# Performance work log

Hardware: AMD Instinct MI355X
Metric: run time of the kernel (lower is better)

## Reference

```python
import jax, jax.numpy as jnp
import numpy as np

N = 50000
E = 400000
IN_DIM = 256
HID = 64
HEADS = 8
OUT_DIM = 40
NEG_SLOPE = 0.2  # PyG GATConv leaky-relu slope


def gat_conv(x, src, dst, W, a_src, a_dst, bias, concat):
    """One PyG-style GATConv (eval mode, self-loops already appended).
    x: [N, in], W: [in, H*C], a_src/a_dst: [H, C], bias: [H*C] or [C]."""
    H, C = a_src.shape
    h = (x @ W).reshape(N, H, C)                       # [N, H, C]
    # per-node attention logits, gathered per edge
    e_src = (h * a_src[None]).sum(-1)                  # [N, H]
    e_dst = (h * a_dst[None]).sum(-1)                  # [N, H]
    alpha = jax.nn.leaky_relu(e_src[src] + e_dst[dst], NEG_SLOPE)  # [Etot, H]
    # segment softmax over incoming edges of each dst node
    amax = jax.ops.segment_max(alpha, dst, num_segments=N)         # [N, H]
    ex = jnp.exp(alpha - amax[dst])
    denom = jax.ops.segment_sum(ex, dst, num_segments=N)           # [N, H]
    coef = ex / denom[dst]                                         # [Etot, H]
    # weighted scatter-add of neighbor features
    msg = h[src] * coef[:, :, None]                                # [Etot, H, C]
    out = jax.ops.segment_sum(msg, dst, num_segments=N)            # [N, H, C]
    out = out.reshape(N, H * C) if concat else out.mean(axis=1)
    return out + bias


def setup_inputs() -> dict:
    key = jax.random.key(0)
    ks = jax.random.split(key, 10)
    x = jax.random.normal(ks[0], (N, IN_DIM), dtype=jnp.float32)
    edge_index = jax.random.randint(ks[1], (2, E), 0, N, dtype=jnp.int32)
    g1 = 1.0 / np.sqrt(IN_DIM)
    g2 = 1.0 / np.sqrt(HID * HEADS)
    W1 = jax.random.normal(ks[2], (IN_DIM, HEADS * HID), dtype=jnp.float32) * g1
    a_src1 = jax.random.normal(ks[3], (HEADS, HID), dtype=jnp.float32) * 0.1
    a_dst1 = jax.random.normal(ks[4], (HEADS, HID), dtype=jnp.float32) * 0.1
    b1 = jnp.zeros((HEADS * HID,), dtype=jnp.float32)
    W2 = jax.random.normal(ks[5], (HEADS * HID, OUT_DIM), dtype=jnp.float32) * g2
    a_src2 = jax.random.normal(ks[6], (1, OUT_DIM), dtype=jnp.float32) * 0.1
    a_dst2 = jax.random.normal(ks[7], (1, OUT_DIM), dtype=jnp.float32) * 0.1
    b2 = jnp.zeros((OUT_DIM,), dtype=jnp.float32)
    return {"x": x, "edge_index": edge_index, "W1": W1, "a_src1": a_src1,
            "a_dst1": a_dst1, "b1": b1, "W2": W2, "a_src2": a_src2,
            "a_dst2": a_dst2, "b2": b2}


def reference(x, edge_index, W1, a_src1, a_dst1, b1, W2, a_src2, a_dst2, b2):
    # append self loops (PyG GATConv default add_self_loops=True)
    loop = jnp.arange(N, dtype=edge_index.dtype)
    src = jnp.concatenate([edge_index[0], loop])
    dst = jnp.concatenate([edge_index[1], loop])
    h = gat_conv(x, src, dst, W1, a_src1, a_dst1, b1, concat=True)
    h = jax.nn.elu(h)
    # dropout is identity in eval mode
    out = gat_conv(h, src, dst, W2, a_src2, a_dst2, b2, concat=False)
    return out
```

## Files before the change

### kernel.cpp

```cpp
#include <hip/hip_runtime.h>
#include <hip/hip_bf16.h>
#include <math.h>

#define IN_DIM 256
#define HEADS 8
#define HID 64
#define HC1 512
#define OUT_DIM 40
#define NEG_SLOPE 0.2f

typedef __attribute__((ext_vector_type(8))) short short8;
typedef __attribute__((ext_vector_type(4))) float f32x4;

__device__ __forceinline__ unsigned short f2b(float f) {
    __hip_bfloat16 h = __float2bfloat16(f);
    unsigned short u;
    __builtin_memcpy(&u, &h, 2);
    return u;
}

#define LRELU(a) ((a) > 0.f ? (a) : NEG_SLOPE * (a))

#define NB_W ((HC1 * IN_DIM + 48 * HC1 + 255) / 256)

__global__ __launch_bounds__(256) void prologue_kernel(
    const float* __restrict__ W1, const float* __restrict__ W2,
    __hip_bfloat16* __restrict__ W1T, __hip_bfloat16* __restrict__ W2T,
    const int* __restrict__ ei, int* __restrict__ deg, int E, int ET)
{
    int b = blockIdx.x;
    if (b < NB_W) {
        int i = b * 256 + threadIdx.x;
        if (i < HC1 * IN_DIM) {
            int n = i >> 8, k = i & 255;
            W1T[i] = __float2bfloat16(W1[(size_t)k * HC1 + n]);
        }
        int j = i - HC1 * IN_DIM;
        if (j >= 0 && j < 48 * HC1) {
            int n = j >> 9, k = j & 511;
            W2T[j] = __float2bfloat16(n < OUT_DIM ? W2[(size_t)k * OUT_DIM + n] : 0.f);
        }
    } else {
        int e = (b - NB_W) * 256 + threadIdx.x;
        if (e >= ET) return;
        int d = (e < E) ? ei[E + e] : e - E;
        atomicAdd(&deg[d], 1);
    }
}


__global__ __launch_bounds__(256) void scan1_kernel(
    const int* __restrict__ deg, int* __restrict__ rowptr,
    int* __restrict__ aux, int N)
{
    __shared__ int sd[256];
    int tid = threadIdx.x;
    int i = blockIdx.x * 256 + tid;
    int v = (i < N) ? deg[i] : 0;
    sd[tid] = v;
    __syncthreads();
    for (int off = 1; off < 256; off <<= 1) {
        int t = (tid >= off) ? sd[tid - off] : 0;
        __syncthreads();
        sd[tid] += t;
        __syncthreads();
    }
    if (i < N) rowptr[i] = sd[tid] - v;
    if (tid == 255) aux[blockIdx.x] = sd[255];
}

__global__ __launch_bounds__(256) void scan_finish_kernel(
    int* __restrict__ rowptr, int* __restrict__ cursor,
    const int* __restrict__ aux, int N, int ET)
{
    __shared__ int sd[256];
    int tid = threadIdx.x;
    sd[tid] = (tid < blockIdx.x) ? aux[tid] : 0;
    __syncthreads();
#pragma unroll
    for (int off = 128; off > 0; off >>= 1) {
        if (tid < off) sd[tid] += sd[tid + off];
        __syncthreads();
    }
    int prefix = sd[0];
    int i = blockIdx.x * 256 + tid;
    if (i < N) {
        int v = rowptr[i] + prefix;
        rowptr[i] = v;
        cursor[i] = v;
    }
    if (i == 0) rowptr[N] = ET;
}

__global__ __launch_bounds__(512) void gemm1_build(
    const float* __restrict__ x, const __hip_bfloat16* __restrict__ W1T,
    const float* __restrict__ a_src1, const float* __restrict__ a_dst1,
    __hip_bfloat16* __restrict__ h1, float* __restrict__ e_src1,
    float* __restrict__ e_dst1,
    const int* __restrict__ ei, int* __restrict__ cursor,
    int* __restrict__ csr_src, int buildBlocks, int E, int ET, int N)
{
    if ((int)blockIdx.x < buildBlocks) {
        int e = blockIdx.x * 512 + threadIdx.x;
        if (e < ET) {
            int s, d;
            if (e < E) { s = ei[e]; d = ei[E + e]; } else { s = d = e - E; }
            int pos = atomicAdd(&cursor[d], 1);
            csr_src[pos] = s;
        }
        return;
    }

    __shared__ __hip_bfloat16 As[64][264];
    const int tid = threadIdx.x;
    const int row0 = (blockIdx.x - buildBlocks) * 64;

    {
        int rr = tid >> 3;
        int cb = (tid & 7) * 32;
        int rowc = row0 + rr; if (rowc >= N) rowc = N - 1;
        const float* xp = x + (size_t)rowc * IN_DIM + cb;
#pragma unroll
        for (int j = 0; j < 4; ++j) {
            float4 a0 = *(const float4*)(xp + 8 * j);
            float4 a1 = *(const float4*)(xp + 8 * j + 4);
            short8 v;
            v[0] = f2b(a0.x); v[1] = f2b(a0.y); v[2] = f2b(a0.z); v[3] = f2b(a0.w);
            v[4] = f2b(a1.x); v[5] = f2b(a1.y); v[6] = f2b(a1.z); v[7] = f2b(a1.w);
            *(short8*)(&As[rr][cb + 8 * j]) = v;
        }
    }
    __syncthreads();

    const int w = tid >> 6;
    const int lane = tid & 63;
    const int r = lane & 15, g = lane >> 4;

    f32x4 acc[4][4] = {};
    const short* bp = (const short*)W1T + (size_t)(w * 64 + r) * IN_DIM + 8 * g;

#pragma unroll 2
    for (int kk = 0; kk < IN_DIM; kk += 32) {
        short8 af[4];
#pragma unroll
        for (int rt = 0; rt < 4; ++rt)
            af[rt] = *(const short8*)(&As[rt * 16 + r][kk + 8 * g]);
        short8 bf[4];
#pragma unroll
        for (int t = 0; t < 4; ++t)
            bf[t] = *(const short8*)(bp + (size_t)t * 16 * IN_DIM + kk);
#pragma unroll
        for (int t = 0; t < 4; ++t)
#pragma unroll
            for (int rt = 0; rt < 4; ++rt)
                acc[rt][t] = __builtin_amdgcn_mfma_f32_16x16x32_bf16(
                    af[rt], bf[t], acc[rt][t], 0, 0, 0);
    }

#pragma unroll
    for (int rt = 0; rt < 4; ++rt)
#pragma unroll
        for (int t = 0; t < 4; ++t) {
            int c = w * 64 + t * 16 + r;
#pragma unroll
            for (int q = 0; q < 4; ++q) {
                int row = row0 + rt * 16 + 4 * g + q;
                if (row < N)
                    h1[(size_t)row * HC1 + c] = __float2bfloat16(acc[rt][t][q]);
            }
        }

    float a1v[4], a2v[4];
#pragma unroll
    for (int t = 0; t < 4; ++t) {
        a1v[t] = a_src1[w * 64 + t * 16 + r];
        a2v[t] = a_dst1[w * 64 + t * 16 + r];
    }
#pragma unroll
    for (int rt = 0; rt < 4; ++rt) {
        float ps[4] = {}, pd[4] = {};
#pragma unroll
        for (int t = 0; t < 4; ++t)
#pragma unroll
            for (int q = 0; q < 4; ++q) {
                ps[q] += acc[rt][t][q] * a1v[t];
                pd[q] += acc[rt][t][q] * a2v[t];
            }
#pragma unroll
        for (int off = 1; off < 16; off <<= 1)
#pragma unroll
            for (int q = 0; q < 4; ++q) {
                ps[q] += __shfl_xor(ps[q], off);
                pd[q] += __shfl_xor(pd[q], off);
            }
        if (r == 0) {
#pragma unroll
            for (int q = 0; q < 4; ++q) {
                int row = row0 + rt * 16 + 4 * g + q;
                if (row < N) {
                    e_src1[row * 8 + w] = ps[q];
                    e_dst1[row * 8 + w] = pd[q];
                }
            }
        }
    }
}

__global__ __launch_bounds__(256) void gather1_kernel(
    const int* __restrict__ rowptr, const int* __restrict__ csr_src,
    const __hip_bfloat16* __restrict__ h1, const float* __restrict__ e_src,
    const float* __restrict__ e_dst, const float* __restrict__ b1,
    __hip_bfloat16* __restrict__ hmid, int N)
{
    int d = blockIdx.x * 4 + (threadIdx.x >> 6);
    if (d >= N) return;
    const int lane = threadIdx.x & 63;
    const int h0 = lane >> 3;
    const int base = rowptr[d];
    const int deg = rowptr[d + 1] - base;
    const float edv = e_dst[d * 8 + (lane & 7)];

    float acc[8] = {};
    float ssum = 0.f;

    const int nch = (deg + 7) >> 3;
    for (int c = 0; c < nch; ++c) {
        int i = c * 8 + (lane >> 3);
        int ii = i < deg ? i : deg - 1;
        int s = csr_src[base + ii];
        float v = e_src[s * 8 + (lane & 7)] + edv;
        float coef = (i < deg) ? __expf(LRELU(v)) : 0.f;

        int emax = deg - c * 8; if (emax > 8) emax = 8;
        for (int e = 0; e < emax; ++e) {
            float ce = __shfl(coef, e * 8 + h0);
            int se = __shfl(s, e * 8);
            uint4 u = *(const uint4*)(h1 + ((size_t)se << 9) + 8 * lane);
            acc[0] += ce * __uint_as_float(u.x << 16);
            acc[1] += ce * __uint_as_float(u.x & 0xffff0000u);
            acc[2] += ce * __uint_as_float(u.y << 16);
            acc[3] += ce * __uint_as_float(u.y & 0xffff0000u);
            acc[4] += ce * __uint_as_float(u.z << 16);
            acc[5] += ce * __uint_as_float(u.z & 0xffff0000u);
            acc[6] += ce * __uint_as_float(u.w << 16);
            acc[7] += ce * __uint_as_float(u.w & 0xffff0000u);
            ssum += ce;
        }
    }

    float inv = 1.f / ssum;
    float4 b0 = *(const float4*)(b1 + 8 * lane);
    float4 b4 = *(const float4*)(b1 + 8 * lane + 4);
    float ob[8];
    ob[0] = acc[0] * inv + b0.x; ob[1] = acc[1] * inv + b0.y;
    ob[2] = acc[2] * inv + b0.z; ob[3] = acc[3] * inv + b0.w;
    ob[4] = acc[4] * inv + b4.x; ob[5] = acc[5] * inv + b4.y;
    ob[6] = acc[6] * inv + b4.z; ob[7] = acc[7] * inv + b4.w;
    unsigned short rr[8];
#pragma unroll
    for (int j = 0; j < 8; ++j) {
        float o = ob[j];
        o = o > 0.f ? o : expm1f(o);
        rr[j] = f2b(o);
    }
    *(uint4*)(hmid + (size_t)d * HC1 + 8 * lane) = *(uint4*)rr;
}

__global__ __launch_bounds__(256) void gemm2_mfma(
    const __hip_bfloat16* __restrict__ hmid, const __hip_bfloat16* __restrict__ W2T,
    const float* __restrict__ a_src2, const float* __restrict__ a_dst2,
    __hip_bfloat16* __restrict__ h2, float* __restrict__ e_src2,
    float* __restrict__ e_dst2, int N)
{
    __shared__ __hip_bfloat16 Bs[48][520];
    const int tid = threadIdx.x;

    {
        const short* wp = (const short*)W2T;
#pragma unroll
        for (int i = 0; i < 12; ++i) {
            int idx = tid + i * 256;
            int row = idx >> 6, ch = idx & 63;
            *(short8*)(&Bs[row][ch * 8]) = *(const short8*)(wp + (size_t)row * HC1 + ch * 8);
        }
    }
    __syncthreads();

    const int w = tid >> 6;
    const int lane = tid & 63;
    const int r = lane & 15, g = lane >> 4;
    const int rowW = blockIdx.x * 64 + w * 16;

    int arow = rowW + r; if (arow >= N) arow = N - 1;
    const short* ap = (const short*)hmid + (size_t)arow * HC1 + 8 * g;

    f32x4 acc[3] = {};
#pragma unroll 4
    for (int kk = 0; kk < HC1; kk += 32) {
        short8 af = *(const short8*)(ap + kk);
        short8 bf[3];
#pragma unroll
        for (int t = 0; t < 3; ++t)
            bf[t] = *(const short8*)(&Bs[t * 16 + r][kk + 8 * g]);
#pragma unroll
        for (int t = 0; t < 3; ++t)
            acc[t] = __builtin_amdgcn_mfma_f32_16x16x32_bf16(af, bf[t], acc[t], 0, 0, 0);
    }

#pragma unroll
    for (int t = 0; t < 3; ++t) {
        int c = t * 16 + r;
        if (c < OUT_DIM) {
#pragma unroll
            for (int q = 0; q < 4; ++q) {
                int row = rowW + 4 * g + q;
                if (row < N) h2[(size_t)row * OUT_DIM + c] = __float2bfloat16(acc[t][q]);
            }
        }
    }

    float as[3], ad[3];
#pragma unroll
    for (int t = 0; t < 3; ++t) {
        int c = t * 16 + r;
        as[t] = (c < OUT_DIM) ? a_src2[c] : 0.f;
        ad[t] = (c < OUT_DIM) ? a_dst2[c] : 0.f;
    }
    float ps[4] = {}, pd[4] = {};
#pragma unroll
    for (int t = 0; t < 3; ++t)
#pragma unroll
        for (int q = 0; q < 4; ++q) {
            ps[q] += acc[t][q] * as[t];
            pd[q] += acc[t][q] * ad[t];
        }
#pragma unroll
    for (int off = 1; off < 16; off <<= 1)
#pragma unroll
        for (int q = 0; q < 4; ++q) {
            ps[q] += __shfl_xor(ps[q], off);
            pd[q] += __shfl_xor(pd[q], off);
        }
    if (r == 0) {
#pragma unroll
        for (int q = 0; q < 4; ++q) {
            int row = rowW + 4 * g + q;
            if (row < N) { e_src2[row] = ps[q]; e_dst2[row] = pd[q]; }
        }
    }
}

__global__ __launch_bounds__(256) void gather2_kernel(
    const int* __restrict__ rowptr, const int* __restrict__ csr_src,
    const __hip_bfloat16* __restrict__ h2, const float* __restrict__ e_src,
    const float* __restrict__ e_dst, const float* __restrict__ b2,
    float* __restrict__ out, int N)
{
    int wid = (blockIdx.x * blockDim.x + threadIdx.x) >> 6;
    if (wid >= N) return;
    int lane = threadIdx.x & 63;
    int base = rowptr[wid], end = rowptr[wid + 1];
    float ed = e_dst[wid];
    bool act = lane < OUT_DIM;
    int ln = act ? lane : 0;
    const unsigned short* h2u = (const unsigned short*)h2;

    float acc = 0.f, ssum = 0.f;
    int j = base;
    for (; j + 4 <= end; j += 4) {
        int s0 = csr_src[j], s1 = csr_src[j + 1], s2 = csr_src[j + 2], s3 = csr_src[j + 3];
        float v0 = e_src[s0] + ed, v1 = e_src[s1] + ed;
        float v2 = e_src[s2] + ed, v3 = e_src[s3] + ed;
        unsigned f0 = h2u[(size_t)s0 * OUT_DIM + ln];
        unsigned f1 = h2u[(size_t)s1 * OUT_DIM + ln];
        unsigned f2 = h2u[(size_t)s2 * OUT_DIM + ln];
        unsigned f3 = h2u[(size_t)s3 * OUT_DIM + ln];
        float e0 = __expf(LRELU(v0)), e1 = __expf(LRELU(v1));
        float e2 = __expf(LRELU(v2)), e3 = __expf(LRELU(v3));
        acc += e0 * __uint_as_float(f0 << 16) + e1 * __uint_as_float(f1 << 16)
             + e2 * __uint_as_float(f2 << 16) + e3 * __uint_as_float(f3 << 16);
        ssum += e0 + e1 + e2 + e3;
    }
    for (; j < end; ++j) {
        int s0 = csr_src[j];
        float v0 = e_src[s0] + ed;
        unsigned f0 = h2u[(size_t)s0 * OUT_DIM + ln];
        float e0 = __expf(LRELU(v0));
        acc += e0 * __uint_as_float(f0 << 16);
        ssum += e0;
    }
    if (act)
        out[(size_t)wid * OUT_DIM + lane] = acc / ssum + b2[lane];
}

extern "C" void kernel_launch(void* const* d_in, const int* in_sizes, int n_in,
                              void* d_out, int out_size, void* d_ws, size_t ws_size,
                              hipStream_t stream)
{
    const float* x      = (const float*)d_in[0];
    const int*   ei     = (const int*)d_in[1];
    const float* W1     = (const float*)d_in[2];
    const float* a_src1 = (const float*)d_in[3];
    const float* a_dst1 = (const float*)d_in[4];
    const float* b1     = (const float*)d_in[5];
    const float* W2     = (const float*)d_in[6];
    const float* a_src2 = (const float*)d_in[7];
    const float* a_dst2 = (const float*)d_in[8];
    const float* b2     = (const float*)d_in[9];
    float* out = (float*)d_out;

    const int N  = in_sizes[0] / IN_DIM;
    const int E  = in_sizes[1] / 2;
    const int ET = E + N;

    char* p = (char*)d_ws;
    auto alloc = [&](size_t bytes) -> void* {
        void* r = (void*)p;
        p += (bytes + 255) & ~(size_t)255;
        return r;
    };
    __hip_bfloat16* h1b    = (__hip_bfloat16*)alloc((size_t)N * HC1 * 2);
    __hip_bfloat16* hmid   = (__hip_bfloat16*)alloc((size_t)N * HC1 * 2);
    __hip_bfloat16* h2     = (__hip_bfloat16*)alloc((size_t)N * OUT_DIM * 2);
    float*    e_src1  = (float*)alloc((size_t)N * HEADS * 4);
    float*    e_dst1  = (float*)alloc((size_t)N * HEADS * 4);
    float*    e_src2  = (float*)alloc((size_t)N * 4);
    float*    e_dst2  = (float*)alloc((size_t)N * 4);
    int*      deg     = (int*)alloc((size_t)N * 4);
    int*      rowptr  = (int*)alloc((size_t)(N + 1) * 4);
    int*      cursor  = (int*)alloc((size_t)N * 4);
    int*      csr_src = (int*)alloc((size_t)ET * 4);
    int*      aux     = (int*)alloc(256 * 4);
    __hip_bfloat16* W1T = (__hip_bfloat16*)alloc((size_t)HC1 * IN_DIM * 2);
    __hip_bfloat16* W2T = (__hip_bfloat16*)alloc((size_t)48 * HC1 * 2);

    const int nbN    = (N + 255) / 256;
    const int nbET   = (ET + 255) / 256;
    const int nbB512 = (ET + 511) / 512;
    const int nbG    = (N + 63) / 64;

    hipMemsetAsync(deg, 0, (size_t)N * 4, stream);
    prologue_kernel<<<NB_W + nbET, 256, 0, stream>>>(W1, W2, W1T, W2T, ei, deg, E, ET);

    scan1_kernel<<<nbN, 256, 0, stream>>>(deg, rowptr, aux, N);
    scan_finish_kernel<<<nbN, 256, 0, stream>>>(rowptr, cursor, aux, N, ET);

    gemm1_build<<<nbB512 + nbG, 512, 0, stream>>>(x, W1T, a_src1, a_dst1, h1b,
                                                  e_src1, e_dst1, ei, cursor,
                                                  csr_src, nbB512, E, ET, N);
    gather1_kernel<<<(N + 3) / 4, 256, 0, stream>>>(rowptr, csr_src, h1b, e_src1,
                                                    e_dst1, b1, hmid, N);

    gemm2_mfma<<<(N + 63) / 64, 256, 0, stream>>>(hmid, W2T, a_src2, a_dst2, h2,
                                                  e_src2, e_dst2, N);
    gather2_kernel<<<(N + 3) / 4, 256, 0, stream>>>(rowptr, csr_src, h2, e_src2,
                                                    e_dst2, b2, out, N);
}
```

Before: 222.9 us.

## Split layer-1 GEMM by head halves and interleave with CSR build and gather

Layer-1 work is split into two head halves. The first GEMM half shares a launch with the CSR edge build. The second half shares a launch with the gather for heads 0-3, and a final kernel gathers heads 4-7. The first GEMM pass also writes a bf16 copy of x, so the second pass skips the fp32-to-bf16 conversion. The aim is to overlap compute-bound MFMA blocks with memory-bound scatter and gather blocks in the same launch. In exchange it adds a bf16 x buffer write and read, reads CSR indices and attention logits twice, and depends on interleaved block scheduling actually achieving overlap.

```diff
diff --git a/kernel.cpp b/kernel.cpp
--- a/kernel.cpp
+++ b/kernel.cpp
@@ -92,52 +92,48 @@
     if (i == 0) rowptr[N] = ET;
 }
 
-__global__ __launch_bounds__(512) void gemm1_build(
-    const float* __restrict__ x, const __hip_bfloat16* __restrict__ W1T,
+template <int HOFF, bool FROM_XB>
+__device__ __forceinline__ void gemm1_body(
+    int row0, int tid, __hip_bfloat16 (*As)[264],
+    const float* __restrict__ x, __hip_bfloat16* __restrict__ xb,
+    const __hip_bfloat16* __restrict__ W1T,
     const float* __restrict__ a_src1, const float* __restrict__ a_dst1,
     __hip_bfloat16* __restrict__ h1, float* __restrict__ e_src1,
-    float* __restrict__ e_dst1,
-    const int* __restrict__ ei, int* __restrict__ cursor,
-    int* __restrict__ csr_src, int buildBlocks, int E, int ET, int N)
-{
-    if ((int)blockIdx.x < buildBlocks) {
-        int e = blockIdx.x * 512 + threadIdx.x;
-        if (e < ET) {
-            int s, d;
-            if (e < E) { s = ei[e]; d = ei[E + e]; } else { s = d = e - E; }
-            int pos = atomicAdd(&cursor[d], 1);
-            csr_src[pos] = s;
-        }
-        return;
-    }
-
-    __shared__ __hip_bfloat16 As[64][264];
-    const int tid = threadIdx.x;
-    const int row0 = (blockIdx.x - buildBlocks) * 64;
-
+    float* __restrict__ e_dst1, int N)
+{
     {
-        int rr = tid >> 3;
-        int cb = (tid & 7) * 32;
+        int rr = tid >> 2;
+        int cb = (tid & 3) * 64;
         int rowc = row0 + rr; if (rowc >= N) rowc = N - 1;
-        const float* xp = x + (size_t)rowc * IN_DIM + cb;
-#pragma unroll
-        for (int j = 0; j < 4; ++j) {
-            float4 a0 = *(const float4*)(xp + 8 * j);
-            float4 a1 = *(const float4*)(xp + 8 * j + 4);
-            short8 v;
-            v[0] = f2b(a0.x); v[1] = f2b(a0.y); v[2] = f2b(a0.z); v[3] = f2b(a0.w);
-            v[4] = f2b(a1.x); v[5] = f2b(a1.y); v[6] = f2b(a1.z); v[7] = f2b(a1.w);
-            *(short8*)(&As[rr][cb + 8 * j]) = v;
+        if (FROM_XB) {
+            const short* xp = (const short*)xb + (size_t)rowc * IN_DIM + cb;
+#pragma unroll
+            for (int j = 0; j < 8; ++j)
+                *(short8*)(&As[rr][cb + 8 * j]) = *(const short8*)(xp + 8 * j);
+        } else {
+            const float* xp = x + (size_t)rowc * IN_DIM + cb;
+            short* xbp = (short*)xb + (size_t)rowc * IN_DIM + cb;
+#pragma unroll
+            for (int j = 0; j < 8; ++j) {
+                float4 a0 = *(const float4*)(xp + 8 * j);
+                float4 a1 = *(const float4*)(xp + 8 * j + 4);
+                short8 v;
+                v[0] = f2b(a0.x); v[1] = f2b(a0.y); v[2] = f2b(a0.z); v[3] = f2b(a0.w);
+                v[4] = f2b(a1.x); v[5] = f2b(a1.y); v[6] = f2b(a1.z); v[7] = f2b(a1.w);
+                *(short8*)(&As[rr][cb + 8 * j]) = v;
+                *(short8*)(xbp + 8 * j) = v;
+            }
         }
     }
     __syncthreads();
 
     const int w = tid >> 6;
+    const int head = HOFF + w;
     const int lane = tid & 63;
     const int r = lane & 15, g = lane >> 4;
 
     f32x4 acc[4][4] = {};
-    const short* bp = (const short*)W1T + (size_t)(w * 64 + r) * IN_DIM + 8 * g;
+    const short* bp = (const short*)W1T + (size_t)(head * 64 + r) * IN_DIM + 8 * g;
 
 #pragma unroll 2
     for (int kk = 0; kk < IN_DIM; kk += 32) {
@@ -161,7 +157,7 @@
     for (int rt = 0; rt < 4; ++rt)
 #pragma unroll
         for (int t = 0; t < 4; ++t) {
-            int c = w * 64 + t * 16 + r;
+            int c = head * 64 + t * 16 + r;
 #pragma unroll
             for (int q = 0; q < 4; ++q) {
                 int row = row0 + rt * 16 + 4 * g + q;
@@ -173,8 +169,8 @@
     float a1v[4], a2v[4];
 #pragma unroll
     for (int t = 0; t < 4; ++t) {
-        a1v[t] = a_src1[w * 64 + t * 16 + r];
-        a2v[t] = a_dst1[w * 64 + t * 16 + r];
+        a1v[t] = a_src1[head * 64 + t * 16 + r];
+        a2v[t] = a_dst1[head * 64 + t * 16 + r];
     }
 #pragma unroll
     for (int rt = 0; rt < 4; ++rt) {
@@ -198,44 +194,48 @@
             for (int q = 0; q < 4; ++q) {
                 int row = row0 + rt * 16 + 4 * g + q;
                 if (row < N) {
-                    e_src1[row * 8 + w] = ps[q];
-                    e_dst1[row * 8 + w] = pd[q];
+                    e_src1[row * 8 + head] = ps[q];
+                    e_dst1[row * 8 + head] = pd[q];
                 }
             }
         }
     }
 }
 
-__global__ __launch_bounds__(256) void gather1_kernel(
+template <int HOFF>
+__device__ __forceinline__ void gather1_body(
+    int nodeBase, int tid,
     const int* __restrict__ rowptr, const int* __restrict__ csr_src,
     const __hip_bfloat16* __restrict__ h1, const float* __restrict__ e_src,
     const float* __restrict__ e_dst, const float* __restrict__ b1,
     __hip_bfloat16* __restrict__ hmid, int N)
 {
-    int d = blockIdx.x * 4 + (threadIdx.x >> 6);
+    const int lane = tid & 63;
+    const int sl = lane & 31, up = lane & 32;
+    const int d = nodeBase + ((tid >> 6) << 1) + (lane >> 5);
     if (d >= N) return;
-    const int lane = threadIdx.x & 63;
-    const int h0 = lane >> 3;
     const int base = rowptr[d];
     const int deg = rowptr[d + 1] - base;
-    const float edv = e_dst[d * 8 + (lane & 7)];
+    const int hc = HOFF + (sl & 3);
+    const float edv = e_dst[d * 8 + hc];
+    const int h0 = sl >> 3;
+    const int c0 = HOFF * 64 + 8 * sl;
 
     float acc[8] = {};
     float ssum = 0.f;
-
     const int nch = (deg + 7) >> 3;
     for (int c = 0; c < nch; ++c) {
-        int i = c * 8 + (lane >> 3);
+        int i = c * 8 + (sl >> 2);
         int ii = i < deg ? i : deg - 1;
         int s = csr_src[base + ii];
-        float v = e_src[s * 8 + (lane & 7)] + edv;
+        float v = e_src[(size_t)s * 8 + hc] + edv;
         float coef = (i < deg) ? __expf(LRELU(v)) : 0.f;
 
         int emax = deg - c * 8; if (emax > 8) emax = 8;
         for (int e = 0; e < emax; ++e) {
-            float ce = __shfl(coef, e * 8 + h0);
-            int se = __shfl(s, e * 8);
-            uint4 u = *(const uint4*)(h1 + ((size_t)se << 9) + 8 * lane);
+            float ce = __shfl(coef, up + e * 4 + h0);
+            int se = __shfl(s, up + e * 4);
+            uint4 u = *(const uint4*)(h1 + ((size_t)se << 9) + c0);
             acc[0] += ce * __uint_as_float(u.x << 16);
             acc[1] += ce * __uint_as_float(u.x & 0xffff0000u);
             acc[2] += ce * __uint_as_float(u.y << 16);
@@ -249,8 +249,8 @@
     }
 
     float inv = 1.f / ssum;
-    float4 b0 = *(const float4*)(b1 + 8 * lane);
-    float4 b4 = *(const float4*)(b1 + 8 * lane + 4);
+    float4 b0 = *(const float4*)(b1 + c0);
+    float4 b4 = *(const float4*)(b1 + c0 + 4);
     float ob[8];
     ob[0] = acc[0] * inv + b0.x; ob[1] = acc[1] * inv + b0.y;
     ob[2] = acc[2] * inv + b0.z; ob[3] = acc[3] * inv + b0.w;
@@ -263,7 +263,69 @@
         o = o > 0.f ? o : expm1f(o);
         rr[j] = f2b(o);
     }
-    *(uint4*)(hmid + (size_t)d * HC1 + 8 * lane) = *(uint4*)rr;
+    *(uint4*)(hmid + (size_t)d * HC1 + c0) = *(uint4*)rr;
+}
+
+__global__ __launch_bounds__(256) void k3_gemm1A_build(
+    const float* __restrict__ x, __hip_bfloat16* __restrict__ xb,
+    const __hip_bfloat16* __restrict__ W1T,
+    const float* __restrict__ a_src1, const float* __restrict__ a_dst1,
+    __hip_bfloat16* __restrict__ h1, float* __restrict__ e_src1,
+    float* __restrict__ e_dst1,
+    const int* __restrict__ ei, int* __restrict__ cursor,
+    int* __restrict__ csr_src, int NG1, int E, int ET, int N)
+{
+    __shared__ __hip_bfloat16 As[64][264];
+    int b = blockIdx.x;
+    int g = b / 3;
+    if ((b % 3) == 0 && g < NG1) {
+        gemm1_body<0, false>(g * 64, threadIdx.x, As, x, xb, W1T, a_src1, a_dst1,
+                             h1, e_src1, e_dst1, N);
+    } else {
+        int nge = (b + 2) / 3; if (nge > NG1) nge = NG1;
+        int bi = b - nge;
+        int e = bi * 256 + threadIdx.x;
+        if (e < ET) {
+            int s, d;
+            if (e < E) { s = ei[e]; d = ei[E + e]; } else { s = d = e - E; }
+            int pos = atomicAdd(&cursor[d], 1);
+            csr_src[pos] = s;
+        }
+    }
+}
+
+__global__ __launch_bounds__(256) void k4_gemm1B_gather1A(
+    const float* __restrict__ x, __hip_bfloat16* __restrict__ xb,
+    const __hip_bfloat16* __restrict__ W1T,
+    const float* __restrict__ a_src1, const float* __restrict__ a_dst1,
+    __hip_bfloat16* __restrict__ h1, float* __restrict__ e_src1,
+    float* __restrict__ e_dst1,
+    const int* __restrict__ rowptr, const int* __restrict__ csr_src,
+    const float* __restrict__ b1, __hip_bfloat16* __restrict__ hmid,
+    int NG1, int N)
+{
+    __shared__ __hip_bfloat16 As[64][264];
+    int b = blockIdx.x;
+    int g = b / 9;
+    if ((b % 9) == 0 && g < NG1) {
+        gemm1_body<4, true>(g * 64, threadIdx.x, As, x, xb, W1T, a_src1, a_dst1,
+                            h1, e_src1, e_dst1, N);
+    } else {
+        int nge = (b + 8) / 9; if (nge > NG1) nge = NG1;
+        int gi = b - nge;
+        gather1_body<0>(gi * 8, threadIdx.x, rowptr, csr_src, h1, e_src1,
+                        e_dst1, b1, hmid, N);
+    }
+}
+
+__global__ __launch_bounds__(256) void k5_gather1B(
+    const int* __restrict__ rowptr, const int* __restrict__ csr_src,
+    const __hip_bfloat16* __restrict__ h1, const float* __restrict__ e_src,
+    const float* __restrict__ e_dst, const float* __restrict__ b1,
+    __hip_bfloat16* __restrict__ hmid, int N)
+{
+    gather1_body<4>(blockIdx.x * 8, threadIdx.x, rowptr, csr_src, h1, e_src,
+                    e_dst, b1, hmid, N);
 }
 
 __global__ __launch_bounds__(256) void gemm2_mfma(
@@ -422,6 +484,7 @@
     __hip_bfloat16* h1b    = (__hip_bfloat16*)alloc((size_t)N * HC1 * 2);
     __hip_bfloat16* hmid   = (__hip_bfloat16*)alloc((size_t)N * HC1 * 2);
     __hip_bfloat16* h2     = (__hip_bfloat16*)alloc((size_t)N * OUT_DIM * 2);
+    __hip_bfloat16* xb     = (__hip_bfloat16*)alloc((size_t)N * IN_DIM * 2);
     float*    e_src1  = (float*)alloc((size_t)N * HEADS * 4);
     float*    e_dst1  = (float*)alloc((size_t)N * HEADS * 4);
     float*    e_src2  = (float*)alloc((size_t)N * 4);
@@ -436,8 +499,13 @@
 
     const int nbN    = (N + 255) / 256;
     const int nbET   = (ET + 255) / 256;
-    const int nbB512 = (ET + 511) / 512;
-    const int nbG    = (N + 63) / 64;
+    const int NG1    = (N + 63) / 64;
+    const int NGATH  = (N + 7) / 8;
+
+    int T3 = NG1 + nbET;
+    if (T3 < 3 * NG1 - 2) T3 = 3 * NG1 - 2;
+    int T4 = NG1 + NGATH;
+    if (T4 < 9 * NG1 - 8) T4 = 9 * NG1 - 8;
 
     hipMemsetAsync(deg, 0, (size_t)N * 4, stream);
     prologue_kernel<<<NB_W + nbET, 256, 0, stream>>>(W1, W2, W1T, W2T, ei, deg, E, ET);
@@ -445,11 +513,16 @@
     scan1_kernel<<<nbN, 256, 0, stream>>>(deg, rowptr, aux, N);
     scan_finish_kernel<<<nbN, 256, 0, stream>>>(rowptr, cursor, aux, N, ET);
 
-    gemm1_build<<<nbB512 + nbG, 512, 0, stream>>>(x, W1T, a_src1, a_dst1, h1b,
-                                                  e_src1, e_dst1, ei, cursor,
-                                                  csr_src, nbB512, E, ET, N);
-    gather1_kernel<<<(N + 3) / 4, 256, 0, stream>>>(rowptr, csr_src, h1b, e_src1,
-                                                    e_dst1, b1, hmid, N);
+    k3_gemm1A_build<<<T3, 256, 0, stream>>>(x, xb, W1T, a_src1, a_dst1, h1b,
+                                            e_src1, e_dst1, ei, cursor, csr_src,
+                                            NG1, E, ET, N);
+
+    k4_gemm1B_gather1A<<<T4, 256, 0, stream>>>(x, xb, W1T, a_src1, a_dst1, h1b,
+                                               e_src1, e_dst1, rowptr, csr_src,
+                                               b1, hmid, NG1, N);
+
+    k5_gather1B<<<NGATH, 256, 0, stream>>>(rowptr, csr_src, h1b, e_src1,
+                                           e_dst1, b1, hmid, N);
 
     gemm2_mfma<<<(N + 63) / 64, 256, 0, stream>>>(hmid, W2T, a_src2, a_dst2, h2,
                                                   e_src2, e_dst2, N);
```

Result: slower. 294.9 us (+32.3%).
